# Performance work log

Hardware: AMD Instinct MI355X
Metric: run time of the kernel (lower is better)

Reference implementation:

```python
import jax, jax.numpy as jnp
import numpy as np

B, L, H, NH, NE, M = 4, 1024, 768, 12, 42, 8
EMB = 768
OFFSET = 1  # bert cls offset


def setup_inputs() -> dict:
    key = jax.random.key(0)
    ks = jax.random.split(key, 6)
    seq = jax.random.normal(ks[0], (B, L, H), jnp.float32)
    attn = jax.random.uniform(ks[1], (B, NH, L, L), jnp.float32)
    attn = attn / attn.sum(-1, keepdims=True)  # row-stochastic like softmaxed attention probs
    W_head = jax.random.normal(ks[2], (2 * H, EMB), jnp.float32) * 0.02
    b_head = jnp.zeros((EMB,), jnp.float32)
    W_tail = jax.random.normal(ks[3], (2 * H, EMB), jnp.float32) * 0.02
    b_tail = jnp.zeros((EMB,), jnp.float32)
    # mention start positions (before +offset); keep start+offset < L
    mention_pos = jax.random.randint(ks[4], (B, NE, M), 0, L - OFFSET - 1)
    counts = jax.random.randint(ks[5], (B, NE), 1, M + 1)  # >=1 valid mention per entity
    mention_mask = jnp.arange(M)[None, None, :] < counts[:, :, None]
    return dict(sequence_output=seq, attention=attn, W_head=W_head, b_head=b_head,
                W_tail=W_tail, b_tail=b_tail, mention_pos=mention_pos,
                mention_mask=mention_mask)


def _get_hrt(seq, attn, mention_pos, mention_mask):
    # seq: [B,L,H]; attn: [B,NH,L,L]; mention_pos/mask: [B,NE,M]
    b_idx = jnp.arange(B)[:, None, None]
    pos = mention_pos + OFFSET                          # [B,NE,M]
    m_emb = seq[b_idx, pos]                             # [B,NE,M,H] mention embeddings
    att_t = jnp.transpose(attn, (0, 2, 1, 3))           # [B,L,NH,L]
    m_att = att_t[b_idx, pos]                           # [B,NE,M,NH,L] mention attentions
    mask = mention_mask
    neg_inf = jnp.finfo(seq.dtype).min
    # per-entity logsumexp pooling over mentions
    ent_emb = jax.nn.logsumexp(jnp.where(mask[..., None], m_emb, neg_inf), axis=2)
    has_m = mask.any(axis=2)
    ent_emb = jnp.where(has_m[..., None], ent_emb, 0.0)  # [B,NE,H]
    cnt = mask.sum(axis=2).astype(seq.dtype)
    ent_att = (m_att * mask[..., None, None].astype(seq.dtype)).sum(axis=2)
    ent_att = ent_att / jnp.maximum(cnt, 1.0)[..., None, None]  # [B,NE,NH,L] mean over mentions
    # all ordered (head, tail) pairs on the NE x NE grid
    hs = jnp.broadcast_to(ent_emb[:, :, None, :], (B, NE, NE, H))
    ts = jnp.broadcast_to(ent_emb[:, None, :, :], (B, NE, NE, H))
    # ht_att = relu(mean_h(h_att * t_att)), normalized over seq, then context = ht_att @ seq
    ht = jnp.einsum('bihl,bjhl->bijl', ent_att, ent_att) / NH  # [B,NE,NE,L]
    ht = jax.nn.relu(ht)
    ht = ht / (ht.sum(-1, keepdims=True) + 1e-10)
    rs = jnp.einsum('bijl,bld->bijd', ht, seq)                  # [B,NE,NE,H]
    return hs, rs, ts


def reference(sequence_output, attention, W_head, b_head, W_tail, b_tail, mention_pos, mention_mask):
    hs, rs, ts = _get_hrt(sequence_output, attention, mention_pos, mention_mask)
    h_out = jnp.tanh(jnp.concatenate([hs, rs], axis=-1) @ W_head + b_head)
    t_out = jnp.tanh(jnp.concatenate([ts, rs], axis=-1) @ W_tail + b_tail)
    return h_out, t_out
```

## Files before the change

### kernel.cpp

```cpp
#include <hip/hip_runtime.h>
#include <math.h>

typedef _Float16 f16;
typedef __attribute__((ext_vector_type(4))) _Float16 f16x4;
typedef __attribute__((ext_vector_type(8))) _Float16 f16x8;
typedef __attribute__((ext_vector_type(4))) float f32x4;

#define B_    4
#define L_    1024
#define H_    768
#define NH_   12
#define NE_   42
#define M_    8
#define E2_   1536
#define HTP_  1792
#define OUT_HALF 5419008LL

typedef __attribute__((address_space(1))) const unsigned char ga_t;
typedef __attribute__((address_space(3))) unsigned char la_t;
__device__ __forceinline__ void async16(const void* g, void* l) {
    __builtin_amdgcn_global_load_lds((ga_t*)g, (la_t*)l, 16, 0, 0);
}

__global__ void k_ent_emb(const float* __restrict__ seq,
                          const int* __restrict__ mpos,
                          const int* __restrict__ mmask,
                          f16* __restrict__ ent) {
    int e = blockIdx.x, b = blockIdx.y;
    int tid = threadIdx.x;
    const int* mp = mpos  + (b*NE_ + e)*M_;
    const int* mk = mmask + (b*NE_ + e)*M_;
    int pos[M_], msk[M_];
#pragma unroll
    for (int m = 0; m < M_; m++) { msk[m] = mk[m]; pos[m] = mp[m] + 1; }
#pragma unroll
    for (int q = 0; q < 3; q++) {
        int h = tid + q*256;
        float mx = -1e30f, vals[M_];
#pragma unroll
        for (int m = 0; m < M_; m++) {
            vals[m] = 0.f;
            if (msk[m]) {
                float v = seq[((long long)b*L_ + pos[m])*H_ + h];
                vals[m] = v; mx = fmaxf(mx, v);
            }
        }
        float s = 0.f;
#pragma unroll
        for (int m = 0; m < M_; m++) if (msk[m]) s += expf(vals[m] - mx);
        float lse = (mx > -1e29f) ? mx + logf(s) : 0.f;
        ent[(b*NE_ + e)*H_ + h] = (f16)lse;
    }
}

__global__ void k_ent_att(const float* __restrict__ attn,
                          const int* __restrict__ mpos,
                          const int* __restrict__ mmask,
                          f16* __restrict__ eatt) {
    int nh = blockIdx.x, e = blockIdx.y, b = blockIdx.z;
    int tid = threadIdx.x;
    int l0 = tid * 4;
    const int* mp = mpos  + (b*NE_ + e)*M_;
    const int* mk = mmask + (b*NE_ + e)*M_;
    const float* abase = attn + (long long)(b*NH_ + nh) * L_ * L_;
    f32x4 acc = {0,0,0,0}; int cnt = 0;
#pragma unroll
    for (int m = 0; m < M_; m++) {
        if (mk[m]) {
            cnt++;
            const float* row = abase + (long long)(mp[m] + 1) * L_;
            acc += *(const f32x4*)(row + l0);
        }
    }
    float inv = 1.f / (float)(cnt > 0 ? cnt : 1);
    f16x4 o = {(f16)(acc[0]*inv), (f16)(acc[1]*inv), (f16)(acc[2]*inv), (f16)(acc[3]*inv)};
    *(f16x4*)(eatt + ((long long)(b*NE_ + e)*NH_ + nh)*L_ + l0) = o;
}

__global__ __launch_bounds__(256) void k_ht(const f16* __restrict__ eatt,
                                            f16* __restrict__ HT) {
    int jg = blockIdx.x, i = blockIdx.y, b = blockIdx.z;
    int tid = threadIdx.x;
    __shared__ __align__(16) f16 ei_s[NH_*L_];
    __shared__ float red[4];
    const f16* ei = eatt + (long long)(b*NE_ + i)*NH_*L_;
#pragma unroll
    for (int q = 0; q < 6; q++) {
        int off = (q*256 + tid)*8;
        *(f16x8*)(ei_s + off) = *(const f16x8*)(ei + off);
    }
    __syncthreads();
    int l0 = tid*4;
    int wave = tid >> 6, lane = tid & 63;
    for (int jj = 0; jj < 7; jj++) {
        int j = jg*7 + jj;
        const f16* ej = eatt + (long long)(b*NE_ + j)*NH_*L_;
        f32x4 acc = {0,0,0,0};
#pragma unroll
        for (int h = 0; h < NH_; h++) {
            f16x4 vi = *(const f16x4*)(ei_s + h*L_ + l0);
            f16x4 vj = *(const f16x4*)(ej   + h*L_ + l0);
#pragma unroll
            for (int r = 0; r < 4; r++) acc[r] += (float)vi[r] * (float)vj[r];
        }
        float v[4]; float s = 0.f;
#pragma unroll
        for (int r = 0; r < 4; r++) {
            float t = acc[r] * (1.f/12.f);
            t = t > 0.f ? t : 0.f;
            v[r] = t; s += t;
        }
#pragma unroll
        for (int m = 1; m < 64; m <<= 1) s += __shfl_xor(s, m, 64);
        if (lane == 0) red[wave] = s;
        __syncthreads();
        float S = red[0] + red[1] + red[2] + red[3];
        __syncthreads();
        float sc = 1.f / (S + 1e-10f);
        f16x4 o = {(f16)(v[0]*sc), (f16)(v[1]*sc), (f16)(v[2]*sc), (f16)(v[3]*sc)};
        *(f16x4*)(HT + ((long long)b*HTP_ + i*NE_ + j)*L_ + l0) = o;
    }
}

__global__ __launch_bounds__(256)
void k_prep(const float* __restrict__ Wh, const float* __restrict__ Wt,
            const float* __restrict__ bh, const float* __restrict__ bt,
            f16* __restrict__ wtop, f16* __restrict__ wbot,
            float* __restrict__ bcat) {
    __shared__ float tile[32][33];
    int tx = blockIdx.x, ty = blockIdx.y, m = blockIdx.z;
    const float* src = (m & 1) ? Wt : Wh;
    int roff = (m & 2) ? H_ : 0;
    f16* dst = (m & 2) ? wbot : wtop;
    int coff = (m & 1) ? H_ : 0;
    int x = threadIdx.x & 31, y8 = threadIdx.x >> 5;
#pragma unroll
    for (int r = 0; r < 4; r++) {
        int h = ty*32 + y8 + r*8, c = tx*32 + x;
        tile[y8 + r*8][x] = src[(long long)(roff + h)*H_ + c];
    }
    __syncthreads();
#pragma unroll
    for (int r = 0; r < 4; r++) {
        int c2 = tx*32 + y8 + r*8, h2 = ty*32 + x;
        dst[(long long)(coff + c2)*H_ + h2] = (f16)tile[x][y8 + r*8];
    }
    if (tx == 0 && ty == 0 && m == 0) {
        for (int idx = threadIdx.x; idx < E2_; idx += 256)
            bcat[idx] = (idx < H_) ? bh[idx] : bt[idx - H_];
    }
}

__global__ void k_seq16(const float* __restrict__ seq, f16* __restrict__ seq16) {
    int idx = (blockIdx.x*256 + threadIdx.x) * 4;
    f32x4 v = *(const f32x4*)(seq + idx);
    f16x4 o = {(f16)v[0], (f16)v[1], (f16)v[2], (f16)v[3]};
    *(f16x4*)(seq16 + idx) = o;
}

#define LDSS 40
__global__ __launch_bounds__(256)
void k_gemm_het(const f16* __restrict__ A, const f16* __restrict__ BT,
                int M, int K, float* __restrict__ het, const float* __restrict__ bcat) {
    __shared__ __align__(16) f16 As[64*LDSS];
    __shared__ __align__(16) f16 Bs[64*LDSS];
    int bm = blockIdx.x*64, bn = blockIdx.y*64;
    int tid = threadIdx.x;
    int wave = tid >> 6, lane = tid & 63;
    int wm = (wave >> 1)*32, wn = (wave & 1)*32;
    int lo4 = lane & 15, kq = (lane >> 4)*8;
    int srow = tid >> 2, scol = (tid & 3)*8;
    bool aval = (bm + srow) < M;
    const f16* aptr = A + (long long)(bm + srow)*K + scol;
    const f16* bptr = BT + (long long)(bn + srow)*K + scol;
    f32x4 acc[2][2] = {};
    for (int k0 = 0; k0 < K; k0 += 32) {
        uint4 zero = {0,0,0,0};
        uint4 av = aval ? *(const uint4*)(aptr + k0) : zero;
        uint4 bv = *(const uint4*)(bptr + k0);
        __syncthreads();
        *(uint4*)(As + srow*LDSS + scol) = av;
        *(uint4*)(Bs + srow*LDSS + scol) = bv;
        __syncthreads();
        f16x8 a0 = *(const f16x8*)(As + (wm +      lo4)*LDSS + kq);
        f16x8 a1 = *(const f16x8*)(As + (wm + 16 + lo4)*LDSS + kq);
        f16x8 b0 = *(const f16x8*)(Bs + (wn +      lo4)*LDSS + kq);
        f16x8 b1 = *(const f16x8*)(Bs + (wn + 16 + lo4)*LDSS + kq);
        acc[0][0] = __builtin_amdgcn_mfma_f32_16x16x32_f16(a0, b0, acc[0][0], 0,0,0);
        acc[0][1] = __builtin_amdgcn_mfma_f32_16x16x32_f16(a0, b1, acc[0][1], 0,0,0);
        acc[1][0] = __builtin_amdgcn_mfma_f32_16x16x32_f16(a1, b0, acc[1][0], 0,0,0);
        acc[1][1] = __builtin_amdgcn_mfma_f32_16x16x32_f16(a1, b1, acc[1][1], 0,0,0);
    }
    int rloc = (lane >> 4)*4;
#pragma unroll
    for (int sm = 0; sm < 2; sm++)
#pragma unroll
    for (int sn = 0; sn < 2; sn++) {
        f32x4 a = acc[sm][sn];
        int c  = bn + wn + sn*16 + lo4;
        int rb = bm + wm + sm*16 + rloc;
#pragma unroll
        for (int r = 0; r < 4; r++)
            if (rb + r < M) het[(rb + r)*E2_ + c] = a[r] + bcat[c];
    }
}

template<int MODE>
__global__ __launch_bounds__(256)
void k_gemm2(const f16* __restrict__ A, const f16* __restrict__ BT, int K,
             long long strideA, long long strideBT,
             const float* __restrict__ het, float* __restrict__ outp,
             f16* __restrict__ outp16) {
    __shared__ __align__(16) f16 As[128*32];
    __shared__ __align__(16) f16 Bs[128*32];
    int bm = blockIdx.x*128, bn = blockIdx.y*128, bz = blockIdx.z;
    const f16* Ab = A + strideA*bz;
    const f16* Bb = BT + strideBT*bz;
    int tid = threadIdx.x, wave = tid >> 6, lane = tid & 63;
    int wm = (wave >> 1)*64, wn = (wave & 1)*64;
    int lo4 = lane & 15, kq = (lane >> 4)*8;
    int lrow = lane >> 2, lcol = (lane & 3)*8;
    const f16* ag = Ab + (long long)(bm + wave*32 + lrow)*K + lcol;
    const f16* bg = Bb + (long long)(bn + wave*32 + lrow)*K + lcol;
    f16* asl = As + wave*1024;
    f16* bsl = Bs + wave*1024;
    f32x4 acc[4][4] = {};
    for (int k0 = 0; k0 < K; k0 += 32) {
        async16(ag + k0,          asl);
        async16(ag + k0 + 16*K,   asl + 512);
        async16(bg + k0,          bsl);
        async16(bg + k0 + 16*K,   bsl + 512);
        __syncthreads();
        f16x8 af[4], bf[4];
#pragma unroll
        for (int s = 0; s < 4; s++) {
            af[s] = *(const f16x8*)(As + (wm + s*16 + lo4)*32 + kq);
            bf[s] = *(const f16x8*)(Bs + (wn + s*16 + lo4)*32 + kq);
        }
#pragma unroll
        for (int sm = 0; sm < 4; sm++)
#pragma unroll
        for (int sn = 0; sn < 4; sn++)
            acc[sm][sn] = __builtin_amdgcn_mfma_f32_16x16x32_f16(af[sm], bf[sn], acc[sm][sn], 0,0,0);
        __syncthreads();
    }
    int rloc = (lane >> 4)*4;
#pragma unroll
    for (int sm = 0; sm < 4; sm++)
#pragma unroll
    for (int sn = 0; sn < 4; sn++) {
        f32x4 a = acc[sm][sn];
        int c  = bn + wn + sn*16 + lo4;
        int rb = bm + wm + sm*16 + rloc;
        if constexpr (MODE == 1) {
            f16x4 o = {(f16)a[0], (f16)a[1], (f16)a[2], (f16)a[3]};
            *(f16x4*)(outp16 + (long long)bz*E2_*L_ + (long long)c*L_ + rb) = o;
        } else {
#pragma unroll
            for (int r = 0; r < 4; r++) {
                int row = rb + r;
                if (row < NE_*NE_) {
                    int i = row / NE_;
                    int j = row - i*NE_;
                    int sel = (c < H_) ? i : j;
                    float bias = het[(bz*NE_ + sel)*E2_ + c];
                    float v = tanhf(a[r] + bias);
                    long long o = (c < H_)
                        ? ((long long)((bz*NE_ + i)*NE_ + j))*H_ + c
                        : OUT_HALF + ((long long)((bz*NE_ + i)*NE_ + j))*H_ + (c - H_);
                    outp[o] = v;
                }
            }
        }
    }
}

extern "C" void kernel_launch(void* const* d_in, const int* in_sizes, int n_in,
                              void* d_out, int out_size, void* d_ws, size_t ws_size,
                              hipStream_t stream) {
    const float* seq  = (const float*)d_in[0];
    const float* attn = (const float*)d_in[1];
    const float* Wh   = (const float*)d_in[2];
    const float* bh   = (const float*)d_in[3];
    const float* Wt   = (const float*)d_in[4];
    const float* bt   = (const float*)d_in[5];
    const int* mpos   = (const int*)d_in[6];
    const int* mmask  = (const int*)d_in[7];
    float* out = (float*)d_out;
    char* ws = (char*)d_ws;
    f16*   ent   = (f16*)  (ws + 0);
    f16*   wtop  = (f16*)  (ws + 258048);
    f16*   wbot  = (f16*)  (ws + 2617344);
    float* bcat  = (float*)(ws + 4976640);
    float* het   = (float*)(ws + 4982784);
    f16*   eatt  = (f16*)  (ws + 6014976);
    f16*   seq16 = (f16*)  (ws + 10143744);
    f16*   HT    = (f16*)  (ws + 16435200);
    f16*   seqWT = (f16*)  (ws + 31115264);

    k_prep   <<<dim3(24, 24, 4), 256, 0, stream>>>(Wh, Wt, bh, bt, wtop, wbot, bcat);
    k_ent_emb<<<dim3(NE_, B_), 256, 0, stream>>>(seq, mpos, mmask, ent);
    k_ent_att<<<dim3(NH_, NE_, B_), 256, 0, stream>>>(attn, mpos, mmask, eatt);
    k_ht     <<<dim3(6, NE_, B_), 256, 0, stream>>>(eatt, HT);
    k_seq16  <<<3072, 256, 0, stream>>>(seq, seq16);
    k_gemm_het<<<dim3(3, 24, 1), 256, 0, stream>>>(ent, wtop, 168, 768, het, bcat);
    k_gemm2<1><<<dim3(8, 12, B_), 256, 0, stream>>>(seq16, wbot, 768,
        (long long)L_*H_, 0, nullptr, nullptr, seqWT);
    k_gemm2<2><<<dim3(14, 12, B_), 256, 0, stream>>>(HT, seqWT, 1024,
        (long long)HTP_*L_, (long long)E2_*L_, het, out, nullptr);
}
```

Baseline: 403.6 us.

## Merge eight kernel launches into three dependency-level fused kernels

Independent stages (weight prep, seq fp16 cast, entity embedding pooling, entity attention pooling) are merged into one launch dispatched by block index, and the second level (seq×W GEMM, HT computation, head GEMM) into another, leaving the final GEMM separate. This removes per-launch overhead and kernel-boundary gaps, and lets independent work run concurrently on the GPU. In exchange, shared memory is sized for the largest branch, which can lower occupancy for the small branches, and the mixed block types may load-balance unevenly.

Result: faster. 365.1 us (-9.5%).

```diff
diff --git a/kernel.cpp b/kernel.cpp
--- a/kernel.cpp
+++ b/kernel.cpp
@@ -22,11 +22,49 @@
     __builtin_amdgcn_global_load_lds((ga_t*)g, (la_t*)l, 16, 0, 0);
 }
 
-__global__ void k_ent_emb(const float* __restrict__ seq,
-                          const int* __restrict__ mpos,
-                          const int* __restrict__ mmask,
-                          f16* __restrict__ ent) {
-    int e = blockIdx.x, b = blockIdx.y;
+
+__device__ void prep_body(int bid, char* smem,
+                          const float* __restrict__ Wh, const float* __restrict__ Wt,
+                          const float* __restrict__ bh, const float* __restrict__ bt,
+                          f16* __restrict__ wtop, f16* __restrict__ wbot,
+                          float* __restrict__ bcat) {
+    float (*tile)[33] = (float(*)[33])smem;
+    int tx = bid % 24, ty = (bid / 24) % 24, m = bid / 576;
+    const float* src = (m & 1) ? Wt : Wh;
+    int roff = (m & 2) ? H_ : 0;
+    f16* dst = (m & 2) ? wbot : wtop;
+    int coff = (m & 1) ? H_ : 0;
+    int x = threadIdx.x & 31, y8 = threadIdx.x >> 5;
+#pragma unroll
+    for (int r = 0; r < 4; r++) {
+        int h = ty*32 + y8 + r*8, c = tx*32 + x;
+        tile[y8 + r*8][x] = src[(long long)(roff + h)*H_ + c];
+    }
+    __syncthreads();
+#pragma unroll
+    for (int r = 0; r < 4; r++) {
+        int c2 = tx*32 + y8 + r*8, h2 = ty*32 + x;
+        dst[(long long)(coff + c2)*H_ + h2] = (f16)tile[x][y8 + r*8];
+    }
+    if (bid == 0) {
+        for (int idx = threadIdx.x; idx < E2_; idx += 256)
+            bcat[idx] = (idx < H_) ? bh[idx] : bt[idx - H_];
+    }
+}
+
+__device__ void seq16_body(int bid, const float* __restrict__ seq,
+                           f16* __restrict__ seq16) {
+    int idx = (bid*256 + threadIdx.x) * 4;
+    f32x4 v = *(const f32x4*)(seq + idx);
+    f16x4 o = {(f16)v[0], (f16)v[1], (f16)v[2], (f16)v[3]};
+    *(f16x4*)(seq16 + idx) = o;
+}
+
+__device__ void ent_emb_body(int bid, const float* __restrict__ seq,
+                             const int* __restrict__ mpos,
+                             const int* __restrict__ mmask,
+                             f16* __restrict__ ent) {
+    int e = bid % NE_, b = bid / NE_;
     int tid = threadIdx.x;
     const int* mp = mpos  + (b*NE_ + e)*M_;
     const int* mk = mmask + (b*NE_ + e)*M_;
@@ -53,11 +91,11 @@
     }
 }
 
-__global__ void k_ent_att(const float* __restrict__ attn,
-                          const int* __restrict__ mpos,
-                          const int* __restrict__ mmask,
-                          f16* __restrict__ eatt) {
-    int nh = blockIdx.x, e = blockIdx.y, b = blockIdx.z;
+__device__ void ent_att_body(int bid, const float* __restrict__ attn,
+                             const int* __restrict__ mpos,
+                             const int* __restrict__ mmask,
+                             f16* __restrict__ eatt) {
+    int nh = bid % NH_, e = (bid / NH_) % NE_, b = bid / (NH_*NE_);
     int tid = threadIdx.x;
     int l0 = tid * 4;
     const int* mp = mpos  + (b*NE_ + e)*M_;
@@ -77,12 +115,12 @@
     *(f16x4*)(eatt + ((long long)(b*NE_ + e)*NH_ + nh)*L_ + l0) = o;
 }
 
-__global__ __launch_bounds__(256) void k_ht(const f16* __restrict__ eatt,
-                                            f16* __restrict__ HT) {
-    int jg = blockIdx.x, i = blockIdx.y, b = blockIdx.z;
+__device__ void ht_body(int bid, char* smem, const f16* __restrict__ eatt,
+                        f16* __restrict__ HT) {
+    int jg = bid % 6, i = (bid / 6) % NE_, b = bid / 252;
     int tid = threadIdx.x;
-    __shared__ __align__(16) f16 ei_s[NH_*L_];
-    __shared__ float red[4];
+    f16* ei_s = (f16*)smem;
+    float* red = (float*)(smem + NH_*L_*2);
     const f16* ei = eatt + (long long)(b*NE_ + i)*NH_*L_;
 #pragma unroll
     for (int q = 0; q < 6; q++) {
@@ -122,49 +160,14 @@
     }
 }
 
-__global__ __launch_bounds__(256)
-void k_prep(const float* __restrict__ Wh, const float* __restrict__ Wt,
-            const float* __restrict__ bh, const float* __restrict__ bt,
-            f16* __restrict__ wtop, f16* __restrict__ wbot,
-            float* __restrict__ bcat) {
-    __shared__ float tile[32][33];
-    int tx = blockIdx.x, ty = blockIdx.y, m = blockIdx.z;
-    const float* src = (m & 1) ? Wt : Wh;
-    int roff = (m & 2) ? H_ : 0;
-    f16* dst = (m & 2) ? wbot : wtop;
-    int coff = (m & 1) ? H_ : 0;
-    int x = threadIdx.x & 31, y8 = threadIdx.x >> 5;
-#pragma unroll
-    for (int r = 0; r < 4; r++) {
-        int h = ty*32 + y8 + r*8, c = tx*32 + x;
-        tile[y8 + r*8][x] = src[(long long)(roff + h)*H_ + c];
-    }
-    __syncthreads();
-#pragma unroll
-    for (int r = 0; r < 4; r++) {
-        int c2 = tx*32 + y8 + r*8, h2 = ty*32 + x;
-        dst[(long long)(coff + c2)*H_ + h2] = (f16)tile[x][y8 + r*8];
-    }
-    if (tx == 0 && ty == 0 && m == 0) {
-        for (int idx = threadIdx.x; idx < E2_; idx += 256)
-            bcat[idx] = (idx < H_) ? bh[idx] : bt[idx - H_];
-    }
-}
-
-__global__ void k_seq16(const float* __restrict__ seq, f16* __restrict__ seq16) {
-    int idx = (blockIdx.x*256 + threadIdx.x) * 4;
-    f32x4 v = *(const f32x4*)(seq + idx);
-    f16x4 o = {(f16)v[0], (f16)v[1], (f16)v[2], (f16)v[3]};
-    *(f16x4*)(seq16 + idx) = o;
-}
-
 #define LDSS 40
-__global__ __launch_bounds__(256)
-void k_gemm_het(const f16* __restrict__ A, const f16* __restrict__ BT,
-                int M, int K, float* __restrict__ het, const float* __restrict__ bcat) {
-    __shared__ __align__(16) f16 As[64*LDSS];
-    __shared__ __align__(16) f16 Bs[64*LDSS];
-    int bm = blockIdx.x*64, bn = blockIdx.y*64;
+__device__ void gemm_het_body(int bx, int by, char* smem,
+                              const f16* __restrict__ A, const f16* __restrict__ BT,
+                              float* __restrict__ het, const float* __restrict__ bcat) {
+    const int M = 168, K = 768;
+    f16* As = (f16*)smem;
+    f16* Bs = (f16*)(smem + 64*LDSS*2);
+    int bm = bx*64, bn = by*64;
     int tid = threadIdx.x;
     int wave = tid >> 6, lane = tid & 63;
     int wm = (wave >> 1)*32, wn = (wave & 1)*32;
@@ -206,14 +209,14 @@
 }
 
 template<int MODE>
-__global__ __launch_bounds__(256)
-void k_gemm2(const f16* __restrict__ A, const f16* __restrict__ BT, int K,
-             long long strideA, long long strideBT,
-             const float* __restrict__ het, float* __restrict__ outp,
-             f16* __restrict__ outp16) {
-    __shared__ __align__(16) f16 As[128*32];
-    __shared__ __align__(16) f16 Bs[128*32];
-    int bm = blockIdx.x*128, bn = blockIdx.y*128, bz = blockIdx.z;
+__device__ void gemm2_body(int bx, int by, int bz, char* smem,
+                           const f16* __restrict__ A, const f16* __restrict__ BT, int K,
+                           long long strideA, long long strideBT,
+                           const float* __restrict__ het, float* __restrict__ outp,
+                           f16* __restrict__ outp16) {
+    f16* As = (f16*)smem;
+    f16* Bs = (f16*)(smem + 8192);
+    int bm = bx*128, bn = by*128;
     const f16* Ab = A + strideA*bz;
     const f16* Bb = BT + strideBT*bz;
     int tid = threadIdx.x, wave = tid >> 6, lane = tid & 63;
@@ -273,6 +276,48 @@
             }
         }
     }
+}
+
+__global__ __launch_bounds__(256) void k_L1(
+        const float* __restrict__ seq, const float* __restrict__ attn,
+        const float* __restrict__ Wh, const float* __restrict__ bh,
+        const float* __restrict__ Wt, const float* __restrict__ bt,
+        const int* __restrict__ mpos, const int* __restrict__ mmask,
+        f16* __restrict__ wtop, f16* __restrict__ wbot, float* __restrict__ bcat,
+        f16* __restrict__ seq16, f16* __restrict__ ent, f16* __restrict__ eatt) {
+    __shared__ __align__(16) char smem[4224];
+    int bid = blockIdx.x;
+    if (bid < 2304)       prep_body(bid, smem, Wh, Wt, bh, bt, wtop, wbot, bcat);
+    else if (bid < 5376)  seq16_body(bid - 2304, seq, seq16);
+    else if (bid < 5544)  ent_emb_body(bid - 5376, seq, mpos, mmask, ent);
+    else                  ent_att_body(bid - 5544, attn, mpos, mmask, eatt);
+}
+
+__global__ __launch_bounds__(256) void k_L2(
+        const f16* __restrict__ seq16, const f16* __restrict__ wbot,
+        const f16* __restrict__ ent, const f16* __restrict__ wtop,
+        const float* __restrict__ bcat, const f16* __restrict__ eatt,
+        f16* __restrict__ seqWT, float* __restrict__ het, f16* __restrict__ HT) {
+    __shared__ __align__(16) char smem[24640];
+    int bid = blockIdx.x;
+    if (bid < 384) {
+        int bx = bid & 7, by = (bid >> 3) % 12, bz = bid / 96;
+        gemm2_body<1>(bx, by, bz, smem, seq16, wbot, 768,
+                      (long long)L_*H_, 0, nullptr, nullptr, seqWT);
+    } else if (bid < 1392) {
+        ht_body(bid - 384, smem, eatt, HT);
+    } else {
+        int r = bid - 1392;
+        gemm_het_body(r % 3, r / 3, smem, ent, wtop, het, bcat);
+    }
+}
+
+__global__ __launch_bounds__(256) void k_L3(
+        const f16* __restrict__ HT, const f16* __restrict__ seqWT,
+        const float* __restrict__ het, float* __restrict__ outp) {
+    __shared__ __align__(16) char smem[16384];
+    gemm2_body<2>(blockIdx.x, blockIdx.y, blockIdx.z, smem, HT, seqWT, 1024,
+                  (long long)HTP_*L_, (long long)E2_*L_, het, outp, nullptr);
 }
 
 extern "C" void kernel_launch(void* const* d_in, const int* in_sizes, int n_in,
@@ -298,14 +343,9 @@
     f16*   HT    = (f16*)  (ws + 16435200);
     f16*   seqWT = (f16*)  (ws + 31115264);
 
-    k_prep   <<<dim3(24, 24, 4), 256, 0, stream>>>(Wh, Wt, bh, bt, wtop, wbot, bcat);
-    k_ent_emb<<<dim3(NE_, B_), 256, 0, stream>>>(seq, mpos, mmask, ent);
-    k_ent_att<<<dim3(NH_, NE_, B_), 256, 0, stream>>>(attn, mpos, mmask, eatt);
-    k_ht     <<<dim3(6, NE_, B_), 256, 0, stream>>>(eatt, HT);
-    k_seq16  <<<3072, 256, 0, stream>>>(seq, seq16);
-    k_gemm_het<<<dim3(3, 24, 1), 256, 0, stream>>>(ent, wtop, 168, 768, het, bcat);
-    k_gemm2<1><<<dim3(8, 12, B_), 256, 0, stream>>>(seq16, wbot, 768,
-        (long long)L_*H_, 0, nullptr, nullptr, seqWT);
-    k_gemm2<2><<<dim3(14, 12, B_), 256, 0, stream>>>(HT, seqWT, 1024,
-        (long long)HTP_*L_, (long long)E2_*L_, het, out, nullptr);
-}
+    k_L1<<<7560, 256, 0, stream>>>(seq, attn, Wh, bh, Wt, bt, mpos, mmask,
+                                   wtop, wbot, bcat, seq16, ent, eatt);
+    k_L2<<<1464, 256, 0, stream>>>(seq16, wbot, ent, wtop, bcat, eatt,
+                                   seqWT, het, HT);
+    k_L3<<<dim3(14, 12, B_), 256, 0, stream>>>(HT, seqWT, het, out);
+}
```
